# Performance work log

Measured on AMD Instinct MI355X. Metric: run time of the kernel, lower is better.

## Reference

```python
import jax, jax.numpy as jnp
from jax import lax
import numpy as np

GC_LAMBDA = 0.75
N = 8388608  # chain length (number of graph nodes between source and sink)


def setup_inputs() -> dict:
    key = jax.random.key(0)
    inputs = jax.random.uniform(key, (N,), dtype=jnp.float32)  # probabilities in [0,1)
    return {"inputs": inputs}


def reference(inputs):
    # Min s-t cut of the chain graph == Viterbi DP over binary labels x_i:
    #   E(x) = sum_i [x_i==1 ? (1-p_i) : p_i] + lam * sum_{i>0} [x_i != x_{i-1}]
    # Label 1 <=> node on source side (reachable set) in the min cut.
    lam = jnp.float32(GC_LAMBDA)
    cost0 = inputs          # x_i = 0: cut source->i edge, capacity p_i
    cost1 = 1.0 - inputs    # x_i = 1: cut i->sink edge, capacity 1 - p_i

    def fwd(carry, costs):
        a0, a1 = carry       # best energy ending in state 0 / 1 (renormalized)
        c0, c1 = costs
        from1 = a1 + lam < a0   # best predecessor of current state 0 is state 1
        from0 = a0 + lam < a1   # best predecessor of current state 1 is state 0
        n0 = c0 + jnp.minimum(a0, a1 + lam)
        n1 = c1 + jnp.minimum(a1, a0 + lam)
        m = jnp.minimum(n0, n1)  # keep carries small for fp32 accuracy over long chains
        return (n0 - m, n1 - m), (from1, from0)

    (a0, a1), (from1, from0) = lax.scan(
        fwd, (cost0[0], cost1[0]), (cost0[1:], cost1[1:])
    )
    last = a1 < a0  # label of the final node (True -> 1)

    def bwd(state, chs):
        f1, f0 = chs
        prev = jnp.where(state, ~f0, f1)  # backtrack the argmin pointers
        return prev, prev

    _, states = lax.scan(bwd, last, (from1, from0), reverse=True)
    labels = jnp.concatenate([states, last[None]])  # [N] bool
    return labels.astype(jnp.int32)
```

## Files before the change

kernel.cpp:

```cpp
#include <hip/hip_runtime.h>
#include <stdint.h>


#define LAM 0.75f
constexpr int N_TOTAL = 8388608;
constexpr int SEG = 32;
constexpr int NSEG = N_TOTAL / SEG;
constexpr int NBLK = NSEG / 256;

__device__ __forceinline__ float dstep(float d, float p) {
    float e0 = fminf(fmaxf(d, 0.0f), LAM);
    float e1 = fminf(fmaxf(-d, 0.0f), LAM);
    return (p + e0) - ((1.0f - p) + e1);
}

__device__ float seg0_end(const float* __restrict__ p) {
    float p0 = p[0];
    float a0 = p0, a1 = 1.0f - p0;
    float t0 = fminf(a0, a1 + LAM);
    float t1 = fminf(a1, a0 + LAM);
    float p1 = p[1];
    float d = (p1 + t0) - ((1.0f - p1) + t1);
    for (int i = 2; i < SEG; ++i) d = dstep(d, p[i]);
    return d;
}

union SegU { float4 q[8]; float f[32]; };

__global__ __launch_bounds__(256, 4) void k_main(const float* __restrict__ p,
        uint32_t* __restrict__ bsum, int* __restrict__ blast,
        int* __restrict__ out) {
    __shared__ float s_dh[256];
    __shared__ uint8_t s_ok[256];
    __shared__ uint32_t lev[256];
    __shared__ uint32_t lsg[256];
    __shared__ int lC[256];
    const int t = threadIdx.x;
    const int b = blockIdx.x;
    const int s = b * 256 + t;

    SegU u;
    const float4* g4 = (const float4*)(p + (size_t)s * SEG);
    #pragma unroll
    for (int i = 0; i < 8; ++i) u.q[i] = g4[i];

    float dh = 2.0f, dl = -2.0f;
    #pragma unroll
    for (int i = 0; i < SEG; ++i) {
        float pi = u.f[i];
        dh = dstep(dh, pi);
        dl = dstep(dl, pi);
    }
    s_dh[t] = dh;
    s_ok[t] = (dh == dl) ? 1 : 0;
    __syncthreads();

    float d = 0.0f;
    uint32_t em = 0, gm = 0;
    if (s == 0) {
        float p0 = u.f[0];
        float a0 = p0, a1 = 1.0f - p0;
        bool f1 = (a1 + LAM) < a0;
        bool f0 = (a0 + LAM) < a1;
        em |= (uint32_t)(f1 || f0); gm |= (uint32_t)f1;
        float t0 = fminf(a0, a1 + LAM);
        float t1 = fminf(a1, a0 + LAM);
        float p1 = u.f[1];
        d = (p1 + t0) - ((1.0f - p1) + t1);
        em |= (uint32_t)(fabsf(d) > LAM) << 1;
        gm |= (uint32_t)(d > LAM) << 1;
        #pragma unroll
        for (int i = 2; i < SEG; ++i) {
            d = dstep(d, u.f[i]);
            em |= (uint32_t)(fabsf(d) > LAM) << i;
            gm |= (uint32_t)(d > LAM) << i;
        }
    } else {
        int back = t - 1;
        while (back >= 0 && !s_ok[back]) --back;
        int startSeg;
        if (back >= 0) {
            d = s_dh[back];
            startSeg = b * 256 + back;
        } else {
            int v = b * 256 - 1;
            for (;;) {
                if (v == 0) { d = seg0_end(p); startSeg = 0; break; }
                const float4* gv = (const float4*)(p + (size_t)v * SEG);
                float h = 2.0f, l = -2.0f;
                for (int i = 0; i < 8; ++i) {
                    float4 q = gv[i];
                    h = dstep(h, q.x); l = dstep(l, q.x);
                    h = dstep(h, q.y); l = dstep(l, q.y);
                    h = dstep(h, q.z); l = dstep(l, q.z);
                    h = dstep(h, q.w); l = dstep(l, q.w);
                }
                if (h == l) { d = h; startSeg = v; break; }
                --v;
            }
        }
        for (int v = startSeg + 1; v < s; ++v) {
            const float* sv = p + (size_t)v * SEG;
            for (int i = 0; i < SEG; ++i) d = dstep(d, sv[i]);
        }
        #pragma unroll
        for (int i = 0; i < SEG; ++i) {
            d = dstep(d, u.f[i]);
            em |= (uint32_t)(fabsf(d) > LAM) << i;
            gm |= (uint32_t)(d > LAM) << i;
        }
    }
    if (s == NSEG - 1) {
        em |= 0x80000000u;
        gm = (d > 0.0f) ? (gm | 0x80000000u) : (gm & 0x7FFFFFFFu);
    }
    lev[t] = em;
    lsg[t] = gm;
    __syncthreads();

    {
        int cur = 0;
        for (int v = t + 1; v < 256; ++v) {
            uint32_t evv = lev[v];
            if (evv) { cur = (int)((lsg[v] >> __builtin_ctz(evv)) & 1u); break; }
        }
        lC[t] = cur;
    }
    if (t == 0) {
        uint32_t summ = 0;
        for (int v = 0; v < 256; ++v) {
            uint32_t evv = lev[v];
            if (evv) { summ = 2u | (uint32_t)((lsg[v] >> __builtin_ctz(evv)) & 1u); break; }
        }
        bsum[b] = summ;
    }
    if (t == 1) {
        int lp = -1;
        for (int v = 255; v >= 0; --v) {
            uint32_t evv = lev[v];
            if (evv) { lp = b * 8192 + v * 32 + (31 - __builtin_clz(evv)); break; }
        }
        blast[b] = lp;
    }
    __syncthreads();

    int4* o4 = (int4*)out + (size_t)b * 2048;
    #pragma unroll
    for (int i = 0; i < 8; ++i) {
        int c = i * 256 + t;
        int wl = c >> 3;
        int bb = (c & 7) * 4;
        uint32_t we = lev[wl], wg = lsg[wl];
        int wc = lC[wl];
        int4 r;
        uint32_t m = we >> (bb + 0);
        r.x = m ? (int)((wg >> (bb + 0 + __builtin_ctz(m))) & 1u) : wc;
        m = we >> (bb + 1);
        r.y = m ? (int)((wg >> (bb + 1 + __builtin_ctz(m))) & 1u) : wc;
        m = we >> (bb + 2);
        r.z = m ? (int)((wg >> (bb + 2 + __builtin_ctz(m))) & 1u) : wc;
        m = we >> (bb + 3);
        r.w = m ? (int)((wg >> (bb + 3 + __builtin_ctz(m))) & 1u) : wc;
        o4[c] = r;
    }
}

__global__ __launch_bounds__(256) void k_fixup(const uint32_t* __restrict__ bsum,
        const int* __restrict__ blast, int* __restrict__ out) {
    int b = blockIdx.x * 256 + threadIdx.x;
    int lp = blast[b];
    int start = (lp >= 0) ? (lp + 1) : (b * 8192);
    int end = (b + 1) * 8192;
    if (start >= end) return;
    int c = 0;
    for (int v = b + 1; v < NBLK; ++v) {
        uint32_t sv = bsum[v];
        if (sv & 2u) { c = (int)(sv & 1u); break; }
    }
    for (int i = start; i < end; ++i) out[i] = c;
}

extern "C" void kernel_launch(void* const* d_in, const int* in_sizes, int n_in,
                              void* d_out, int out_size, void* d_ws, size_t ws_size,
                              hipStream_t stream) {
    (void)in_sizes; (void)n_in; (void)out_size; (void)ws_size;
    const float* p = (const float*)d_in[0];
    int* out = (int*)d_out;
    char* ws = (char*)d_ws;
    uint32_t* bsum = (uint32_t*)ws;
    int*      blast = (int*)(ws + (size_t)NBLK * 4);

    k_main<<<dim3(NBLK), dim3(256), 0, stream>>>(p, bsum, blast, out);
    k_fixup<<<dim3(NBLK / 256), dim3(256), 0, stream>>>(bsum, blast, out);
}
```

Before: 87.48 us.

## Resolve block-tail labels in-kernel by walking ahead, dropping fixup kernel

Removes the second fixup kernel and its workspace round-trip. The last thread of each block now prefetches the first 16 probabilities of the next block and continues the DP forward from its own end state until the difference leaves the [-λ,λ] band, which gives the carry label for trailing undecided nodes. Bit selection is also made branchless through a pick_bit helper. This saves a launch and a serial scan over block summaries. The cost is a possible long serial walk by one thread when the band is not exited quickly.

```diff
diff --git a/kernel.cpp b/kernel.cpp
--- a/kernel.cpp
+++ b/kernel.cpp
@@ -25,16 +25,25 @@
     return d;
 }
 
+__device__ __forceinline__ uint32_t pick_bit(uint32_t m, uint32_t wg, int sh,
+                                             uint32_t fallback) {
+    uint32_t mm = m ? m : 1u;
+    int idx = (sh + __builtin_ctz(mm)) & 31;
+    uint32_t hit = (wg >> idx) & 1u;
+    return m ? hit : fallback;
+}
+
 union SegU { float4 q[8]; float f[32]; };
+union WalkU { float4 q[4]; float f[16]; };
 
 __global__ __launch_bounds__(256, 4) void k_main(const float* __restrict__ p,
-        uint32_t* __restrict__ bsum, int* __restrict__ blast,
         int* __restrict__ out) {
     __shared__ float s_dh[256];
     __shared__ uint8_t s_ok[256];
     __shared__ uint32_t lev[256];
     __shared__ uint32_t lsg[256];
     __shared__ int lC[256];
+    __shared__ int s_carry;
     const int t = threadIdx.x;
     const int b = blockIdx.x;
     const int s = b * 256 + t;
@@ -43,6 +52,15 @@
     const float4* g4 = (const float4*)(p + (size_t)s * SEG);
     #pragma unroll
     for (int i = 0; i < 8; ++i) u.q[i] = g4[i];
+
+    WalkU wu;
+    #pragma unroll
+    for (int i = 0; i < 4; ++i) wu.q[i] = make_float4(1.0f, 1.0f, 1.0f, 1.0f);
+    if (t == 255 && b + 1 < NBLK) {
+        const float4* nx = (const float4*)(p + (size_t)(b + 1) * 8192);
+        #pragma unroll
+        for (int i = 0; i < 4; ++i) wu.q[i] = nx[i];
+    }
 
     float dh = 2.0f, dl = -2.0f;
     #pragma unroll
@@ -118,30 +136,43 @@
     lsg[t] = gm;
     __syncthreads();
 
-    {
-        int cur = 0;
-        for (int v = t + 1; v < 256; ++v) {
-            uint32_t evv = lev[v];
-            if (evv) { cur = (int)((lsg[v] >> __builtin_ctz(evv)) & 1u); break; }
-        }
-        lC[t] = cur;
-    }
-    if (t == 0) {
-        uint32_t summ = 0;
-        for (int v = 0; v < 256; ++v) {
-            uint32_t evv = lev[v];
-            if (evv) { summ = 2u | (uint32_t)((lsg[v] >> __builtin_ctz(evv)) & 1u); break; }
-        }
-        bsum[b] = summ;
-    }
-    if (t == 1) {
-        int lp = -1;
-        for (int v = 255; v >= 0; --v) {
-            uint32_t evv = lev[v];
-            if (evv) { lp = b * 8192 + v * 32 + (31 - __builtin_clz(evv)); break; }
-        }
-        blast[b] = lp;
-    }
+    int cur = 0; bool found = false;
+    for (int v = t + 1; v < 256; ++v) {
+        uint32_t evv = lev[v];
+        if (evv) {
+            cur = (int)pick_bit(evv, lsg[v], 0, 0u);
+            found = true;
+            break;
+        }
+    }
+
+    if (t == 255) {
+        int c = 0;
+        if (b + 1 < NBLK) {
+            float dd = d;
+            bool done = false;
+            #pragma unroll
+            for (int i = 0; i < 16; ++i) {
+                if (!done) {
+                    dd = dstep(dd, wu.f[i]);
+                    if (fabsf(dd) > LAM) { c = (dd > LAM) ? 1 : 0; done = true; }
+                }
+            }
+            if (!done) {
+                const int base = (b + 1) * 8192 + 16;
+                const int rem = N_TOTAL - base;
+                for (int k = 0; k < rem; ++k) {
+                    dd = dstep(dd, p[base + k]);
+                    if (fabsf(dd) > LAM) { c = (dd > LAM) ? 1 : 0; done = true; break; }
+                }
+                if (!done) c = (dd > 0.0f) ? 1 : 0;
+            }
+        }
+        s_carry = c;
+    }
+    __syncthreads();
+    if (!found) cur = s_carry;
+    lC[t] = cur;
     __syncthreads();
 
     int4* o4 = (int4*)out + (size_t)b * 2048;
@@ -151,45 +182,22 @@
         int wl = c >> 3;
         int bb = (c & 7) * 4;
         uint32_t we = lev[wl], wg = lsg[wl];
-        int wc = lC[wl];
+        uint32_t wc = (uint32_t)lC[wl];
         int4 r;
-        uint32_t m = we >> (bb + 0);
-        r.x = m ? (int)((wg >> (bb + 0 + __builtin_ctz(m))) & 1u) : wc;
-        m = we >> (bb + 1);
-        r.y = m ? (int)((wg >> (bb + 1 + __builtin_ctz(m))) & 1u) : wc;
-        m = we >> (bb + 2);
-        r.z = m ? (int)((wg >> (bb + 2 + __builtin_ctz(m))) & 1u) : wc;
-        m = we >> (bb + 3);
-        r.w = m ? (int)((wg >> (bb + 3 + __builtin_ctz(m))) & 1u) : wc;
+        r.x = (int)pick_bit(we >> (bb + 0), wg, bb + 0, wc);
+        r.y = (int)pick_bit(we >> (bb + 1), wg, bb + 1, wc);
+        r.z = (int)pick_bit(we >> (bb + 2), wg, bb + 2, wc);
+        r.w = (int)pick_bit(we >> (bb + 3), wg, bb + 3, wc);
         o4[c] = r;
     }
-}
-
-__global__ __launch_bounds__(256) void k_fixup(const uint32_t* __restrict__ bsum,
-        const int* __restrict__ blast, int* __restrict__ out) {
-    int b = blockIdx.x * 256 + threadIdx.x;
-    int lp = blast[b];
-    int start = (lp >= 0) ? (lp + 1) : (b * 8192);
-    int end = (b + 1) * 8192;
-    if (start >= end) return;
-    int c = 0;
-    for (int v = b + 1; v < NBLK; ++v) {
-        uint32_t sv = bsum[v];
-        if (sv & 2u) { c = (int)(sv & 1u); break; }
-    }
-    for (int i = start; i < end; ++i) out[i] = c;
 }
 
 extern "C" void kernel_launch(void* const* d_in, const int* in_sizes, int n_in,
                               void* d_out, int out_size, void* d_ws, size_t ws_size,
                               hipStream_t stream) {
-    (void)in_sizes; (void)n_in; (void)out_size; (void)ws_size;
+    (void)in_sizes; (void)n_in; (void)out_size; (void)d_ws; (void)ws_size;
     const float* p = (const float*)d_in[0];
     int* out = (int*)d_out;
-    char* ws = (char*)d_ws;
-    uint32_t* bsum = (uint32_t*)ws;
-    int*      blast = (int*)(ws + (size_t)NBLK * 4);
-
-    k_main<<<dim3(NBLK), dim3(256), 0, stream>>>(p, bsum, blast, out);
-    k_fixup<<<dim3(NBLK / 256), dim3(256), 0, stream>>>(bsum, blast, out);
-}
+
+    k_main<<<dim3(NBLK), dim3(256), 0, stream>>>(p, out);
+}
```

Result: faster. 85.31 us (median of 2 runs) (-2.5%).
